# Kernel tuning notes

Measured on AMD Instinct MI355X. Metric: run time of the kernel, lower is better.

Reference implementation:

```python
import jax, jax.numpy as jnp
import numpy as np

DIM_IN = 1024
DIM_OUT = 1024
N_HOST = 4096
N_GUEST = 8192


def setup_inputs() -> dict:
    key = jax.random.key(0)
    k1, k2, k3, k4, k5 = jax.random.split(key, 5)
    # kaiming_uniform_ default: bound = sqrt(6 / fan_in) with a=sqrt(5) -> gain=sqrt(2/(1+5)); here approximate with uniform init
    bound = float(np.sqrt(6.0 / DIM_IN) / np.sqrt(3.0))
    features_host = jax.random.normal(k1, (N_HOST, DIM_IN), dtype=jnp.float32)
    features_guests = jax.random.normal(k2, (N_GUEST, DIM_IN), dtype=jnp.float32)
    Q = jax.random.uniform(k3, (DIM_IN, DIM_OUT), dtype=jnp.float32, minval=-bound, maxval=bound)
    K = jax.random.uniform(k4, (DIM_IN, DIM_OUT), dtype=jnp.float32, minval=-bound, maxval=bound)
    V = jax.random.uniform(k5, (DIM_IN, DIM_OUT), dtype=jnp.float32, minval=-bound, maxval=bound)
    return {"features_host": features_host, "features_guests": features_guests, "Q": Q, "K": K, "V": V}


def reference(features_host, features_guests, Q, K, V):
    # query: [N, d_out], key/value: [M, d_out]
    query = features_host @ Q
    key = features_guests @ K
    value = features_guests @ V
    scale = 1.0 / jnp.sqrt(jnp.asarray(DIM_OUT, dtype=query.dtype))
    att = jnp.einsum("nd,md->nm", query, key) * scale  # [N, M]
    attention = jax.nn.softmax(att, axis=1)
    # dropout(p=0.2) is identity in eval mode (deterministic reference)
    return attention @ value  # [N, d_out]
```

## Files before the change

kernel.cpp:

```cpp
#include <hip/hip_runtime.h>
#include <stdint.h>

typedef float f32x4 __attribute__((ext_vector_type(4)));
typedef short bf16x8 __attribute__((ext_vector_type(8)));
typedef unsigned short u16;
typedef u16 u16x4 __attribute__((ext_vector_type(4)));

__device__ __forceinline__ u16 f2bf(float f) {
    union { float f; uint32_t u; } v; v.f = f;
    uint32_t r = v.u + 0x7FFFu + ((v.u >> 16) & 1u);
    return (u16)(r >> 16);
}
__device__ __forceinline__ float bf2f(u16 b) {
    union { uint32_t u; float f; } v; v.u = ((uint32_t)b) << 16;
    return v.f;
}

__device__ __forceinline__ void gload16(u16* lds, const u16* g) {
    __builtin_amdgcn_global_load_lds(
        (const __attribute__((address_space(1))) void*)(uintptr_t)g,
        (__attribute__((address_space(3))) void*)(uint32_t)(uintptr_t)lds,
        16, 0, 0);
}

__device__ __forceinline__ int xcd_map(int bid, int nwg) {
    return (bid & 7) * (nwg >> 3) + (bid >> 3);
}

#define BK 32

__device__ __forceinline__ void gemm256_core(
    const u16* __restrict__ A, const u16* __restrict__ Bt,
    int lda, int ldb, int bm, int bn, int kBeg, int nt,
    u16* lds, f32x4 (&acc)[8][4])
{
    const int tid  = threadIdx.x;
    const int lane = tid & 63;
    const int wid  = tid >> 6;
    const int lr   = lane & 15;
    const int kg   = lane >> 4;
    const int wr   = wid >> 2;
    const int wc   = wid & 3;

    const int sr = tid >> 3;
    const int sc = ((tid & 7) ^ (sr & 7)) * 8;
    const u16* As = A  + (size_t)(bm + sr) * lda + kBeg + sc;
    const u16* Bs = Bt + (size_t)(bn + sr) * ldb + kBeg + sc;
    const int ldsW = wid * 512;

    int arow[8], brow[4], kc[2];
#pragma unroll
    for (int m = 0; m < 8; ++m) arow[m] = wr * 8192 + (m * 16 + lr) * 64;
#pragma unroll
    for (int n = 0; n < 4; ++n)
        brow[n] = 16384 + (wc >> 1) * 8192 + ((wc & 1) * 64 + n * 16 + lr) * 64;
#pragma unroll
    for (int ks = 0; ks < 2; ++ks) kc[ks] = (ks * 32 + kg * 8) ^ ((lr & 7) * 8);

#define STG_A(q, h, t) do { \
        const u16* _s = As + (size_t)((h) * 128) * lda + (t) * 64; \
        gload16(lds + (q) * 32768 + (h) * 8192 + ldsW, _s); \
        gload16(lds + (q) * 32768 + (h) * 8192 + 4096 + ldsW, _s + (size_t)64 * lda); \
    } while (0)
#define STG_B(q, h, t) do { \
        const u16* _s = Bs + (size_t)((h) * 128) * ldb + (t) * 64; \
        gload16(lds + (q) * 32768 + 16384 + (h) * 8192 + ldsW, _s); \
        gload16(lds + (q) * 32768 + 16384 + (h) * 8192 + 4096 + ldsW, _s + (size_t)64 * ldb); \
    } while (0)

    STG_A(0, 0, 0); STG_A(0, 1, 0); STG_B(0, 0, 0); STG_B(0, 1, 0);
    STG_B(1, 0, 1); STG_B(1, 1, 1);
    asm volatile("s_waitcnt vmcnt(4)" ::: "memory");
    __builtin_amdgcn_s_barrier();

    bf16x8 fa[4][2], fb[4][2];
    for (int t = 0; t < nt; ++t) {
        const int p  = t & 1;
        const int pb = p * 32768;

#pragma unroll
        for (int m = 0; m < 4; ++m)
#pragma unroll
            for (int ks = 0; ks < 2; ++ks)
                fa[m][ks] = *(const bf16x8*)&lds[pb + arow[m] + kc[ks]];
#pragma unroll
        for (int n = 0; n < 2; ++n)
#pragma unroll
            for (int ks = 0; ks < 2; ++ks)
                fb[n][ks] = *(const bf16x8*)&lds[pb + brow[n] + kc[ks]];
        if (t + 1 < nt) STG_A(p ^ 1, 0, t + 1);
        __builtin_amdgcn_s_barrier();
        asm volatile("s_waitcnt lgkmcnt(0)" ::: "memory");
        __builtin_amdgcn_sched_barrier(0);
        __builtin_amdgcn_s_setprio(1);
#pragma unroll
        for (int ks = 0; ks < 2; ++ks)
#pragma unroll
            for (int m = 0; m < 4; ++m)
#pragma unroll
                for (int n = 0; n < 2; ++n)
                    acc[m][n] = __builtin_amdgcn_mfma_f32_16x16x32_bf16(fa[m][ks], fb[n][ks], acc[m][n], 0, 0, 0);
        __builtin_amdgcn_s_setprio(0);
        __builtin_amdgcn_s_barrier();

#pragma unroll
        for (int n = 2; n < 4; ++n)
#pragma unroll
            for (int ks = 0; ks < 2; ++ks)
                fb[n][ks] = *(const bf16x8*)&lds[pb + brow[n] + kc[ks]];
        if (t + 1 < nt) STG_A(p ^ 1, 1, t + 1);
        __builtin_amdgcn_s_barrier();
        asm volatile("s_waitcnt lgkmcnt(0)" ::: "memory");
        __builtin_amdgcn_sched_barrier(0);
        __builtin_amdgcn_s_setprio(1);
#pragma unroll
        for (int ks = 0; ks < 2; ++ks)
#pragma unroll
            for (int m = 0; m < 4; ++m)
#pragma unroll
                for (int n = 2; n < 4; ++n)
                    acc[m][n] = __builtin_amdgcn_mfma_f32_16x16x32_bf16(fa[m][ks], fb[n][ks], acc[m][n], 0, 0, 0);
        __builtin_amdgcn_s_setprio(0);
        __builtin_amdgcn_s_barrier();

#pragma unroll
        for (int m = 0; m < 4; ++m)
#pragma unroll
            for (int ks = 0; ks < 2; ++ks)
                fa[m][ks] = *(const bf16x8*)&lds[pb + arow[4 + m] + kc[ks]];
        if (t + 2 < nt) STG_B(p, 0, t + 2);
        __builtin_amdgcn_s_barrier();
        asm volatile("s_waitcnt lgkmcnt(0)" ::: "memory");
        __builtin_amdgcn_sched_barrier(0);
        __builtin_amdgcn_s_setprio(1);
#pragma unroll
        for (int ks = 0; ks < 2; ++ks)
#pragma unroll
            for (int m = 0; m < 4; ++m)
#pragma unroll
                for (int n = 0; n < 2; ++n)
                    acc[4 + m][n] = __builtin_amdgcn_mfma_f32_16x16x32_bf16(fa[m][ks], fb[n][ks], acc[4 + m][n], 0, 0, 0);
        __builtin_amdgcn_s_setprio(0);
        __builtin_amdgcn_s_barrier();

        if (t + 2 < nt) STG_B(p, 1, t + 2);
        __builtin_amdgcn_s_barrier();
        __builtin_amdgcn_s_setprio(1);
#pragma unroll
        for (int ks = 0; ks < 2; ++ks)
#pragma unroll
            for (int m = 0; m < 4; ++m)
#pragma unroll
                for (int n = 2; n < 4; ++n)
                    acc[4 + m][n] = __builtin_amdgcn_mfma_f32_16x16x32_bf16(fa[m][ks], fb[n][ks], acc[4 + m][n], 0, 0, 0);
        __builtin_amdgcn_s_setprio(0);
        if (t + 2 < nt)      asm volatile("s_waitcnt vmcnt(4)" ::: "memory");
        else if (t + 1 < nt) asm volatile("s_waitcnt vmcnt(0)" ::: "memory");
        __builtin_amdgcn_s_barrier();
    }
#undef STG_A
#undef STG_B
}

__global__ __launch_bounds__(512, 2)
void qkt256(const u16* __restrict__ A, const u16* __restrict__ Bt,
            u16* __restrict__ C)
{
    __shared__ u16 lds[65536];
    const int swz = xcd_map(blockIdx.x, 512);
    const int bm = (swz >> 5) * 256;
    const int bn = (swz & 31) * 256;
    f32x4 acc[8][4];
#pragma unroll
    for (int m = 0; m < 8; ++m)
#pragma unroll
        for (int n = 0; n < 4; ++n) acc[m][n] = (f32x4){0.f, 0.f, 0.f, 0.f};
    gemm256_core(A, Bt, 1024, 1024, bm, bn, 0, 16, lds, acc);

    const int lane = threadIdx.x & 63, wid = threadIdx.x >> 6;
    const int lr = lane & 15, kg = lane >> 4, wr = wid >> 2, wc = wid & 3;
#pragma unroll
    for (int m = 0; m < 8; ++m)
#pragma unroll
        for (int n = 0; n < 4; ++n) {
            const int col = bn + wc * 64 + n * 16 + lr;
#pragma unroll
            for (int r = 0; r < 4; ++r) {
                const int row = bm + wr * 128 + m * 16 + kg * 4 + r;
                C[(size_t)row * 8192 + col] = f2bf(acc[m][n][r]);
            }
        }
}

__global__ __launch_bounds__(512, 2)
void pv256(const u16* __restrict__ A, const u16* __restrict__ Bt,
           float* __restrict__ C0, float* __restrict__ C1, float* __restrict__ C2)
{
    __shared__ u16 lds[65536];
    const int swz = xcd_map(blockIdx.x, 192);
    const int z   = swz >> 6;
    const int rem = swz & 63;
    const int bm  = (rem >> 2) * 256;
    const int bn  = (rem & 3) * 256;
    const int kBeg = z * 2752;
    const int nt   = (z == 2) ? 42 : 43;
    float* Cv = (z == 0) ? C0 : (z == 1) ? C1 : C2;

    f32x4 acc[8][4];
#pragma unroll
    for (int m = 0; m < 8; ++m)
#pragma unroll
        for (int n = 0; n < 4; ++n) acc[m][n] = (f32x4){0.f, 0.f, 0.f, 0.f};
    gemm256_core(A, Bt, 8192, 8192, bm, bn, kBeg, nt, lds, acc);

    const int lane = threadIdx.x & 63, wid = threadIdx.x >> 6;
    const int lr = lane & 15, kg = lane >> 4, wr = wid >> 2, wc = wid & 3;
#pragma unroll
    for (int m = 0; m < 8; ++m)
#pragma unroll
        for (int n = 0; n < 4; ++n) {
            const int col = bn + wc * 64 + n * 16 + lr;
#pragma unroll
            for (int r = 0; r < 4; ++r) {
                const int row = bm + wr * 128 + m * 16 + kg * 4 + r;
                Cv[(size_t)row * 1024 + col] = acc[m][n][r];
            }
        }
}

__global__ __launch_bounds__(256)
void proj_gemm(const u16* __restrict__ host_bf, const u16* __restrict__ guests_bf,
               const u16* __restrict__ Qt, const u16* __restrict__ Kt,
               const u16* __restrict__ Vt,
               u16* __restrict__ query_bf, u16* __restrict__ key_bf,
               u16* __restrict__ value_t)
{
    __shared__ u16 a_s[128 * BK];
    __shared__ u16 b_s[128 * BK];
    const int id = xcd_map(blockIdx.x, 1280);

    const u16 *A, *B; u16* Crm = nullptr; int bm, bn; int group;
    if (id < 256)      { group = 0; A = host_bf;   B = Qt; Crm = query_bf; bm = (id >> 3) * 128;         bn = (id & 7) * 128; }
    else if (id < 768) { group = 1; A = guests_bf; B = Kt; Crm = key_bf;   bm = ((id - 256) >> 3) * 128; bn = ((id - 256) & 7) * 128; }
    else               { group = 2; A = guests_bf; B = Vt; Crm = nullptr;  bm = ((id - 768) >> 3) * 128; bn = ((id - 768) & 7) * 128; }

    const int tid  = threadIdx.x;
    const int lane = tid & 63;
    const int wid  = tid >> 6;
    const int lr   = lane & 15;
    const int kg   = lane >> 4;
    const int wm   = (wid >> 1) * 64;
    const int wn   = (wid & 1) * 64;
    const int srow = tid >> 2;
    const int scol = (tid & 3) * 8;

    const u16* Ar0 = A + (size_t)(bm + srow) * 1024 + scol;
    const u16* Ar1 = A + (size_t)(bm + 64 + srow) * 1024 + scol;
    const u16* Br0 = B + (size_t)(bn + srow) * 1024 + scol;
    const u16* Br1 = B + (size_t)(bn + 64 + srow) * 1024 + scol;
    u16* a_d0 = a_s + wid * 512;
    u16* a_d1 = a_s + 2048 + wid * 512;
    u16* b_d0 = b_s + wid * 512;
    u16* b_d1 = b_s + 2048 + wid * 512;

    f32x4 acc[4][4];
#pragma unroll
    for (int i = 0; i < 4; ++i)
#pragma unroll
        for (int j = 0; j < 4; ++j)
            acc[i][j] = (f32x4){0.f, 0.f, 0.f, 0.f};

    for (int k0 = 0; k0 < 1024; k0 += BK) {
        __syncthreads();
        gload16(a_d0, Ar0 + k0);
        gload16(a_d1, Ar1 + k0);
        gload16(b_d0, Br0 + k0);
        gload16(b_d1, Br1 + k0);
        __syncthreads();

        bf16x8 af[4], bfr[4];
#pragma unroll
        for (int i = 0; i < 4; ++i)
            af[i] = *(const bf16x8*)&a_s[(wm + i * 16 + lr) * BK + kg * 8];
#pragma unroll
        for (int j = 0; j < 4; ++j)
            bfr[j] = *(const bf16x8*)&b_s[(wn + j * 16 + lr) * BK + kg * 8];
#pragma unroll
        for (int i = 0; i < 4; ++i)
#pragma unroll
            for (int j = 0; j < 4; ++j)
                acc[i][j] = __builtin_amdgcn_mfma_f32_16x16x32_bf16(af[i], bfr[j], acc[i][j], 0, 0, 0);
    }

    const int r0 = kg * 4;
    if (group == 2) {
#pragma unroll
        for (int i = 0; i < 4; ++i) {
#pragma unroll
            for (int j = 0; j < 4; ++j) {
                const int col = bn + wn + j * 16 + lr;
                const int row = bm + wm + i * 16 + r0;
                u16x4 w;
#pragma unroll
                for (int r = 0; r < 4; ++r) w[r] = f2bf(acc[i][j][r]);
                *(u16x4*)&value_t[(size_t)col * 8192 + row] = w;
            }
        }
    } else {
        const float scale = (group == 0) ? 0.03125f : 1.0f;
#pragma unroll
        for (int i = 0; i < 4; ++i) {
#pragma unroll
            for (int j = 0; j < 4; ++j) {
                const int col = bn + wn + j * 16 + lr;
#pragma unroll
                for (int r = 0; r < 4; ++r) {
                    const int row = bm + wm + i * 16 + r0 + r;
                    Crm[(size_t)row * 1024 + col] = f2bf(acc[i][j][r] * scale);
                }
            }
        }
    }
}

__global__ __launch_bounds__(256)
void wtrans(const float* __restrict__ Qw, const float* __restrict__ Kw,
            const float* __restrict__ Vw, u16* __restrict__ Qt,
            u16* __restrict__ Kt, u16* __restrict__ Vt)
{
    __shared__ u16 tile[64][65];
    const float* in = (blockIdx.z == 0) ? Qw : (blockIdx.z == 1) ? Kw : Vw;
    u16* out        = (blockIdx.z == 0) ? Qt : (blockIdx.z == 1) ? Kt : Vt;
    const int r0 = blockIdx.y * 64;
    const int c0 = blockIdx.x * 64;
    const int tr = threadIdx.x >> 2;
    const int tq = threadIdx.x & 3;

    const float* p = in + (size_t)(r0 + tr) * 1024 + c0 + tq * 16;
#pragma unroll
    for (int i = 0; i < 16; i += 4) {
        float4 v = *(const float4*)(p + i);
        tile[tq * 16 + i + 0][tr] = f2bf(v.x);
        tile[tq * 16 + i + 1][tr] = f2bf(v.y);
        tile[tq * 16 + i + 2][tr] = f2bf(v.z);
        tile[tq * 16 + i + 3][tr] = f2bf(v.w);
    }
    __syncthreads();

    u16 tmp[16];
#pragma unroll
    for (int i = 0; i < 16; ++i) tmp[i] = tile[tr][tq * 16 + i];
    bf16x8 w0, w1;
#pragma unroll
    for (int j = 0; j < 8; ++j) { w0[j] = (short)tmp[j]; w1[j] = (short)tmp[8 + j]; }
    u16* o = out + (size_t)(c0 + tr) * 1024 + r0 + tq * 16;
    *(bf16x8*)o       = w0;
    *(bf16x8*)(o + 8) = w1;
}

__global__ __launch_bounds__(256)
void cvt_inputs(const float* __restrict__ host, const float* __restrict__ guests,
                u16* __restrict__ host_bf, u16* __restrict__ guests_bf)
{
    int b = blockIdx.x;
    const float* in; u16* out;
    if (b < 2048) { in = host; out = host_bf; }
    else          { in = guests; out = guests_bf; b -= 2048; }
    const size_t i = ((size_t)b * 256 + threadIdx.x) * 8;
    float4 v0 = *(const float4*)(in + i);
    float4 v1 = *(const float4*)(in + i + 4);
    bf16x8 w;
    w[0] = (short)f2bf(v0.x); w[1] = (short)f2bf(v0.y);
    w[2] = (short)f2bf(v0.z); w[3] = (short)f2bf(v0.w);
    w[4] = (short)f2bf(v1.x); w[5] = (short)f2bf(v1.y);
    w[6] = (short)f2bf(v1.z); w[7] = (short)f2bf(v1.w);
    *(bf16x8*)(out + i) = w;
}

__global__ __launch_bounds__(256)
void add2_f32(float* __restrict__ out, const float* __restrict__ p1,
              const float* __restrict__ p2)
{
    const size_t i = ((size_t)blockIdx.x * 256 + threadIdx.x) * 4;
    float4 a = *(const float4*)(out + i);
    float4 b = *(const float4*)(p1 + i);
    float4 c = *(const float4*)(p2 + i);
    a.x += b.x + c.x; a.y += b.y + c.y; a.z += b.z + c.z; a.w += b.w + c.w;
    *(float4*)(out + i) = a;
}

__global__ __launch_bounds__(256)
void softmax_inplace(u16* __restrict__ att)
{
    const int tid = threadIdx.x;
    u16* p = att + (size_t)blockIdx.x * 8192;

    float x[32];
#pragma unroll
    for (int c = 0; c < 4; ++c) {
        bf16x8 v = *(const bf16x8*)(p + c * 2048 + tid * 8);
#pragma unroll
        for (int j = 0; j < 8; ++j) x[c * 8 + j] = bf2f((u16)v[j]);
    }

    float mx = -1e30f;
#pragma unroll
    for (int i = 0; i < 32; ++i) mx = fmaxf(mx, x[i]);
#pragma unroll
    for (int o = 32; o >= 1; o >>= 1) mx = fmaxf(mx, __shfl_xor(mx, o));

    __shared__ float red[8];
    const int wid = tid >> 6, lane = tid & 63;
    if (lane == 0) red[wid] = mx;
    __syncthreads();
    mx = fmaxf(fmaxf(red[0], red[1]), fmaxf(red[2], red[3]));

    float s = 0.f;
#pragma unroll
    for (int i = 0; i < 32; ++i) { x[i] = __expf(x[i] - mx); s += x[i]; }
#pragma unroll
    for (int o = 32; o >= 1; o >>= 1) s += __shfl_xor(s, o);
    if (lane == 0) red[4 + wid] = s;
    __syncthreads();
    s = red[4] + red[5] + red[6] + red[7];
    const float inv = 1.0f / s;

#pragma unroll
    for (int c = 0; c < 4; ++c) {
        bf16x8 w;
#pragma unroll
        for (int j = 0; j < 8; ++j) w[j] = (short)f2bf(x[c * 8 + j] * inv);
        *(bf16x8*)(p + c * 2048 + tid * 8) = w;
    }
}

extern "C" void kernel_launch(void* const* d_in, const int* in_sizes, int n_in,
                              void* d_out, int out_size, void* d_ws, size_t ws_size,
                              hipStream_t stream)
{
    const float* host   = (const float*)d_in[0];
    const float* guests = (const float*)d_in[1];
    const float* Qw     = (const float*)d_in[2];
    const float* Kw     = (const float*)d_in[3];
    const float* Vw     = (const float*)d_in[4];
    float* out = (float*)d_out;

    char* ws = (char*)d_ws;
    u16* att       = (u16*)(ws);
    u16* host_bf   = (u16*)(ws);
    u16* guests_bf = (u16*)(ws + ( 8ull << 20));
    u16* Qt        = (u16*)(ws + (24ull << 20));
    u16* Kt        = (u16*)(ws + (26ull << 20));
    u16* Vt        = (u16*)(ws + (28ull << 20));
    u16* query_bf  = (u16*)(ws + (64ull << 20));
    u16* key_bf    = (u16*)(ws + (72ull << 20));
    u16* value_t   = (u16*)(ws + (88ull << 20));
    float* part1   = (float*)(ws + (64ull << 20));
    float* part2   = (float*)(ws + (104ull << 20));

    dim3 blk(256);

    cvt_inputs<<<dim3(6144), blk, 0, stream>>>(host, guests, host_bf, guests_bf);
    wtrans<<<dim3(16, 16, 3), blk, 0, stream>>>(Qw, Kw, Vw, Qt, Kt, Vt);

    proj_gemm<<<dim3(1280), blk, 0, stream>>>(host_bf, guests_bf, Qt, Kt, Vt,
                                              query_bf, key_bf, value_t);

    qkt256<<<dim3(512), dim3(512), 0, stream>>>(query_bf, key_bf, att);

    softmax_inplace<<<dim3(4096), blk, 0, stream>>>(att);

    pv256<<<dim3(192), dim3(512), 0, stream>>>(att, value_t, out, part1, part2);
    add2_f32<<<dim3(4096), blk, 0, stream>>>(out, part1, part2);
}
```

Measured before the change: 350.1 us.

## Fuse input prep kernels and split PV GEMM K four ways when workspace allows

The bf16 conversion kernel and the weight-transpose kernel are merged into one launch, which removes a kernel launch boundary. When the workspace is at least 128 MiB, the PV GEMM is split along K into four chunks instead of three. That gives 256 blocks instead of 192, so more of the CUs are busy. This needs a third fp32 partial buffer, a rearranged workspace layout, and an extra read in the final reduction kernel.

```diff
diff --git a/kernel.cpp b/kernel.cpp
--- a/kernel.cpp
+++ b/kernel.cpp
@@ -194,17 +194,19 @@
 
 __global__ __launch_bounds__(512, 2)
 void pv256(const u16* __restrict__ A, const u16* __restrict__ Bt,
-           float* __restrict__ C0, float* __restrict__ C1, float* __restrict__ C2)
+           float* __restrict__ C0, float* __restrict__ C1,
+           float* __restrict__ C2, float* __restrict__ C3,
+           int ntPerZ, int lastZ)
 {
     __shared__ u16 lds[65536];
-    const int swz = xcd_map(blockIdx.x, 192);
+    const int swz = xcd_map(blockIdx.x, gridDim.x);
     const int z   = swz >> 6;
     const int rem = swz & 63;
     const int bm  = (rem >> 2) * 256;
     const int bn  = (rem & 3) * 256;
-    const int kBeg = z * 2752;
-    const int nt   = (z == 2) ? 42 : 43;
-    float* Cv = (z == 0) ? C0 : (z == 1) ? C1 : C2;
+    const int kBeg = z * ntPerZ * 64;
+    const int nt   = (z == lastZ) ? (128 - lastZ * ntPerZ) : ntPerZ;
+    float* Cv = (z == 0) ? C0 : (z == 1) ? C1 : (z == 2) ? C2 : C3;
 
     f32x4 acc[8][4];
 #pragma unroll
@@ -324,15 +326,36 @@
 }
 
 __global__ __launch_bounds__(256)
-void wtrans(const float* __restrict__ Qw, const float* __restrict__ Kw,
-            const float* __restrict__ Vw, u16* __restrict__ Qt,
-            u16* __restrict__ Kt, u16* __restrict__ Vt)
+void prep(const float* __restrict__ host, const float* __restrict__ guests,
+          const float* __restrict__ Qw, const float* __restrict__ Kw,
+          const float* __restrict__ Vw,
+          u16* __restrict__ host_bf, u16* __restrict__ guests_bf,
+          u16* __restrict__ Qt, u16* __restrict__ Kt, u16* __restrict__ Vt)
 {
     __shared__ u16 tile[64][65];
-    const float* in = (blockIdx.z == 0) ? Qw : (blockIdx.z == 1) ? Kw : Vw;
-    u16* out        = (blockIdx.z == 0) ? Qt : (blockIdx.z == 1) ? Kt : Vt;
-    const int r0 = blockIdx.y * 64;
-    const int c0 = blockIdx.x * 64;
+    int b = blockIdx.x;
+    if (b < 6144) {
+        const float* in; u16* out;
+        if (b < 2048) { in = host; out = host_bf; }
+        else          { in = guests; out = guests_bf; b -= 2048; }
+        const size_t i = ((size_t)b * 256 + threadIdx.x) * 8;
+        float4 v0 = *(const float4*)(in + i);
+        float4 v1 = *(const float4*)(in + i + 4);
+        bf16x8 w;
+        w[0] = (short)f2bf(v0.x); w[1] = (short)f2bf(v0.y);
+        w[2] = (short)f2bf(v0.z); w[3] = (short)f2bf(v0.w);
+        w[4] = (short)f2bf(v1.x); w[5] = (short)f2bf(v1.y);
+        w[6] = (short)f2bf(v1.z); w[7] = (short)f2bf(v1.w);
+        *(bf16x8*)(out + i) = w;
+        return;
+    }
+    b -= 6144;
+    const int zz = b >> 8;
+    const int t8 = b & 255;
+    const float* in = (zz == 0) ? Qw : (zz == 1) ? Kw : Vw;
+    u16* out        = (zz == 0) ? Qt : (zz == 1) ? Kt : Vt;
+    const int r0 = (t8 >> 4) * 64;
+    const int c0 = (t8 & 15) * 64;
     const int tr = threadIdx.x >> 2;
     const int tq = threadIdx.x & 3;
 
@@ -359,33 +382,18 @@
 }
 
 __global__ __launch_bounds__(256)
-void cvt_inputs(const float* __restrict__ host, const float* __restrict__ guests,
-                u16* __restrict__ host_bf, u16* __restrict__ guests_bf)
-{
-    int b = blockIdx.x;
-    const float* in; u16* out;
-    if (b < 2048) { in = host; out = host_bf; }
-    else          { in = guests; out = guests_bf; b -= 2048; }
-    const size_t i = ((size_t)b * 256 + threadIdx.x) * 8;
-    float4 v0 = *(const float4*)(in + i);
-    float4 v1 = *(const float4*)(in + i + 4);
-    bf16x8 w;
-    w[0] = (short)f2bf(v0.x); w[1] = (short)f2bf(v0.y);
-    w[2] = (short)f2bf(v0.z); w[3] = (short)f2bf(v0.w);
-    w[4] = (short)f2bf(v1.x); w[5] = (short)f2bf(v1.y);
-    w[6] = (short)f2bf(v1.z); w[7] = (short)f2bf(v1.w);
-    *(bf16x8*)(out + i) = w;
-}
-
-__global__ __launch_bounds__(256)
-void add2_f32(float* __restrict__ out, const float* __restrict__ p1,
-              const float* __restrict__ p2)
+void addN(float* __restrict__ out, const float* __restrict__ p1,
+          const float* __restrict__ p2, const float* __restrict__ p3, int n3)
 {
     const size_t i = ((size_t)blockIdx.x * 256 + threadIdx.x) * 4;
     float4 a = *(const float4*)(out + i);
     float4 b = *(const float4*)(p1 + i);
     float4 c = *(const float4*)(p2 + i);
     a.x += b.x + c.x; a.y += b.y + c.y; a.z += b.z + c.z; a.w += b.w + c.w;
+    if (n3) {
+        float4 d = *(const float4*)(p3 + i);
+        a.x += d.x; a.y += d.y; a.z += d.z; a.w += d.w;
+    }
     *(float4*)(out + i) = a;
 }
 
@@ -452,16 +460,33 @@
     u16* Qt        = (u16*)(ws + (24ull << 20));
     u16* Kt        = (u16*)(ws + (26ull << 20));
     u16* Vt        = (u16*)(ws + (28ull << 20));
-    u16* query_bf  = (u16*)(ws + (64ull << 20));
-    u16* key_bf    = (u16*)(ws + (72ull << 20));
-    u16* value_t   = (u16*)(ws + (88ull << 20));
-    float* part1   = (float*)(ws + (64ull << 20));
-    float* part2   = (float*)(ws + (104ull << 20));
+
+    const bool big = ws_size >= (128ull << 20);
+    u16 *query_bf, *key_bf, *value_t;
+    float *part1, *part2, *part3;
+    int ntPerZ, lastZ, pvGrid, n3;
+    if (big) {
+        value_t  = (u16*)(ws + (64ull  << 20));
+        query_bf = (u16*)(ws + (80ull  << 20));
+        key_bf   = (u16*)(ws + (88ull  << 20));
+        part1    = (float*)(ws + (80ull  << 20));
+        part2    = (float*)(ws + (96ull  << 20));
+        part3    = (float*)(ws + (112ull << 20));
+        ntPerZ = 32; lastZ = 3; pvGrid = 256; n3 = 1;
+    } else {
+        query_bf = (u16*)(ws + (64ull  << 20));
+        key_bf   = (u16*)(ws + (72ull  << 20));
+        value_t  = (u16*)(ws + (88ull  << 20));
+        part1    = (float*)(ws + (64ull  << 20));
+        part2    = (float*)(ws + (104ull << 20));
+        part3    = part1;
+        ntPerZ = 43; lastZ = 2; pvGrid = 192; n3 = 0;
+    }
 
     dim3 blk(256);
 
-    cvt_inputs<<<dim3(6144), blk, 0, stream>>>(host, guests, host_bf, guests_bf);
-    wtrans<<<dim3(16, 16, 3), blk, 0, stream>>>(Qw, Kw, Vw, Qt, Kt, Vt);
+    prep<<<dim3(6912), blk, 0, stream>>>(host, guests, Qw, Kw, Vw,
+                                         host_bf, guests_bf, Qt, Kt, Vt);
 
     proj_gemm<<<dim3(1280), blk, 0, stream>>>(host_bf, guests_bf, Qt, Kt, Vt,
                                               query_bf, key_bf, value_t);
@@ -470,6 +495,8 @@
 
     softmax_inplace<<<dim3(4096), blk, 0, stream>>>(att);
 
-    pv256<<<dim3(192), dim3(512), 0, stream>>>(att, value_t, out, part1, part2);
-    add2_f32<<<dim3(4096), blk, 0, stream>>>(out, part1, part2);
-}
+    pv256<<<dim3(pvGrid), dim3(512), 0, stream>>>(att, value_t, out,
+                                                  part1, part2, part3,
+                                                  ntPerZ, lastZ);
+    addN<<<dim3(4096), blk, 0, stream>>>(out, part1, part2, part3, n3);
+}
```

Measured after the change: 344.3 us. About the same (-1.7%).
